# Performance work log

Measured on AMD Instinct MI355X. Metric: run time of the kernel, lower is better.

Reference implementation:

```python
import jax, jax.numpy as jnp
import numpy as np

N, E, F, H, C = 50000, 800000, 128, 256, 40
BN_EPS = 1e-5


def setup_inputs() -> dict:
    key = jax.random.key(0)
    ks = jax.random.split(key, 8)
    s = 0.05
    return {
        'x': jax.random.normal(ks[0], (N, F), jnp.float32),
        'edge_index': jax.random.randint(ks[1], (2, E), 0, N),
        'eps1': jnp.zeros((), jnp.float32),
        'W1': jax.random.normal(ks[2], (F, H), jnp.float32) * s,
        'b1': jnp.zeros((H,), jnp.float32),
        'g1': jnp.ones((H,), jnp.float32),
        'be1': jnp.zeros((H,), jnp.float32),
        'W2': jax.random.normal(ks[3], (H, H), jnp.float32) * s,
        'b2': jnp.zeros((H,), jnp.float32),
        'eps2': jnp.zeros((), jnp.float32),
        'W3': jax.random.normal(ks[4], (H, H), jnp.float32) * s,
        'b3': jnp.zeros((H,), jnp.float32),
        'g2': jnp.ones((H,), jnp.float32),
        'be2': jnp.zeros((H,), jnp.float32),
        'W4': jax.random.normal(ks[5], (H, H), jnp.float32) * s,
        'b4': jnp.zeros((H,), jnp.float32),
        'g3': jnp.ones((H,), jnp.float32),
        'be3': jnp.zeros((H,), jnp.float32),
        'Wf': jax.random.normal(ks[6], (H, C), jnp.float32) * s,
        'bf': jnp.zeros((C,), jnp.float32),
    }


def _bn(h, g, b):
    # BatchNorm1d forward with batch statistics (training-mode math, biased var)
    m = jnp.mean(h, axis=0)
    v = jnp.var(h, axis=0)
    return (h - m) * jax.lax.rsqrt(v + BN_EPS) * g + b


def _gin_conv(x, edge_index, eps, Wa, ba, g, be, Wb, bb):
    # GINConv: out = mlp((1+eps)*x + sum_{(src->dst)} x[src])
    src, dst = edge_index[0], edge_index[1]
    agg = jax.ops.segment_sum(x[src], dst, num_segments=x.shape[0])  # [N, d]
    h = (1.0 + eps) * x + agg
    h = jnp.maximum(_bn(h @ Wa + ba, g, be), 0.0)  # Linear-BN-ReLU
    return h @ Wb + bb                              # Linear


def reference(x, edge_index, eps1, W1, b1, g1, be1, W2, b2,
              eps2, W3, b3, g2, be2, W4, b4, g3, be3, Wf, bf):
    h = _gin_conv(x, edge_index, eps1, W1, b1, g1, be1, W2, b2)
    h = jnp.maximum(h, 0.0)  # F.relu (dropout p=0)
    h = _gin_conv(h, edge_index, eps2, W3, b3, g2, be2, W4, b4)
    h = jnp.maximum(_bn(h, g3, be3), 0.0)  # bn2 + relu
    return h @ Wf + bf  # fc -> [N, C]
```

## Files before the change

kernel.cpp:

```cpp
#include <hip/hip_runtime.h>
#include <hip/hip_bf16.h>


#define NN 50000
#define EE 800000
#define FDIM 128
#define HDIM 256
#define CDIM 40
#define BN_EPS 1e-5f

typedef unsigned short u16;
typedef unsigned int u32;
typedef __attribute__((ext_vector_type(8))) short short8;
typedef __attribute__((ext_vector_type(4))) float f32x4;

__device__ __forceinline__ float bflo(u32 u) { return __uint_as_float(u << 16); }
__device__ __forceinline__ float bfhi(u32 u) { return __uint_as_float(u & 0xFFFF0000u); }
__device__ __forceinline__ u16 f2bf(float f) {
  __hip_bfloat16 h = __float2bfloat16(f);
  return *(u16*)&h;
}
__device__ __forceinline__ u32 pack2(float a, float b) {
  return (u32)f2bf(a) | ((u32)f2bf(b) << 16);
}

__global__ void k_hist(const int* __restrict__ ei, int* __restrict__ deg) {
  int e = blockIdx.x * 256 + threadIdx.x;
  if (e < EE) atomicAdd(&deg[ei[EE + e]], 1);
}

__global__ void k_scan_blocks(const int* __restrict__ in, int* __restrict__ partial,
                              int* __restrict__ bsums, int n) {
  __shared__ int s[256];
  int i = blockIdx.x * 256 + threadIdx.x;
  s[threadIdx.x] = (i < n) ? in[i] : 0;
  __syncthreads();
  for (int d = 1; d < 256; d <<= 1) {
    int t = (threadIdx.x >= d) ? s[threadIdx.x - d] : 0;
    __syncthreads();
    s[threadIdx.x] += t;
    __syncthreads();
  }
  if (i < n) partial[i] = s[threadIdx.x];
  if (threadIdx.x == 255) bsums[blockIdx.x] = s[255];
}

__global__ void k_scan_sums(int* __restrict__ bs, int nb) {
  __shared__ int s[256];
  s[threadIdx.x] = (threadIdx.x < nb) ? bs[threadIdx.x] : 0;
  __syncthreads();
  for (int d = 1; d < 256; d <<= 1) {
    int t = (threadIdx.x >= d) ? s[threadIdx.x - d] : 0;
    __syncthreads();
    s[threadIdx.x] += t;
    __syncthreads();
  }
  int ex = (threadIdx.x == 0) ? 0 : s[threadIdx.x - 1];
  if (threadIdx.x < nb) bs[threadIdx.x] = ex;
}

__global__ void k_scan_add(const int* __restrict__ partial, const int* __restrict__ bs,
                           const int* __restrict__ deg,
                           int* __restrict__ rowstart, int* __restrict__ cursor, int n) {
  int i = blockIdx.x * 256 + threadIdx.x;
  if (i < n) {
    int incl = partial[i] + bs[blockIdx.x];
    rowstart[i + 1] = incl;
    cursor[i] = incl - deg[i];
  }
  if (i == 0) rowstart[0] = 0;
}

__global__ void k_scatter(const int* __restrict__ ei, int* __restrict__ cursor,
                          int* __restrict__ sorted_src) {
  int e = blockIdx.x * 256 + threadIdx.x;
  if (e < EE) {
    int dst = ei[EE + e];
    int p = atomicAdd(&cursor[dst], 1);
    sorted_src[p] = ei[e];
  }
}

__global__ void k_cvt_x(const float* __restrict__ x, u16* __restrict__ xb,
                        int* __restrict__ deg, float* __restrict__ stats) {
  int i = blockIdx.x * 256 + threadIdx.x;
  if (i < NN) deg[i] = 0;
  if (i < 6 * 256) stats[i] = 0.f;
  size_t base = (size_t)i * 4;
  if (base < (size_t)NN * FDIM) {
    float4 v = *(const float4*)&x[base];
    *(uint2*)&xb[base] = make_uint2(pack2(v.x, v.y), pack2(v.z, v.w));
  }
}

__global__ void k_cvt_w(const float* __restrict__ W1, const float* __restrict__ W2,
                        const float* __restrict__ W3, const float* __restrict__ W4,
                        const float* __restrict__ Wf,
                        u16* __restrict__ W1t, u16* __restrict__ W2t,
                        u16* __restrict__ W3t, u16* __restrict__ W4t,
                        u16* __restrict__ Wft) {
  int b = blockIdx.x, t = threadIdx.x;
  if (b < 128) {
    int i = b * 256 + t; int k = i >> 8, n = i & 255;
    W1t[(size_t)n * 128 + (((k >> 3) ^ (n & 7)) << 3) + (k & 7)] = f2bf(W1[i]);
  } else if (b < 384) {
    int i = (b - 128) * 256 + t; int k = i >> 8, n = i & 255;
    W2t[(size_t)n * 256 + (((k >> 3) ^ (n & 7)) << 3) + (k & 7)] = f2bf(W2[i]);
  } else if (b < 640) {
    int i = (b - 384) * 256 + t; int k = i >> 8, n = i & 255;
    W3t[(size_t)n * 256 + (((k >> 3) ^ (n & 7)) << 3) + (k & 7)] = f2bf(W3[i]);
  } else if (b < 896) {
    int i = (b - 640) * 256 + t; int k = i >> 8, n = i & 255;
    W4t[(size_t)n * 256 + (((k >> 3) ^ (n & 7)) << 3) + (k & 7)] = f2bf(W4[i]);
  } else {
    int j = (b - 896) * 256 + t;
    int c = j >> 8, k = j & 255;
    float v = (c < CDIM) ? Wf[(size_t)k * CDIM + c] : 0.f;
    Wft[(size_t)c * 256 + (((k >> 3) ^ (c & 7)) << 3) + (k & 7)] = f2bf(v);
  }
}

__global__ __launch_bounds__(256)
void k_agg1(const u16* __restrict__ x, const int* __restrict__ rowstart,
            const int* __restrict__ sorted_src, const float* __restrict__ epsp,
            u16* __restrict__ out) {
  int node = blockIdx.x * 4 + (threadIdx.x >> 6);
  if (node >= NN) return;
  int lane = threadIdx.x & 63;
  float e1 = 1.0f + epsp[0];
  int s = rowstart[node], t = rowstart[node + 1];
  const u32* xp = (const u32*)x;
  u32 u = xp[(size_t)node * 64 + lane];
  float a0 = bflo(u) * e1, a1 = bfhi(u) * e1;
  int p = s;
  for (; p + 7 < t; p += 8) {
    u32 uu[8];
#pragma unroll
    for (int i = 0; i < 8; ++i) uu[i] = xp[(size_t)sorted_src[p + i] * 64 + lane];
#pragma unroll
    for (int i = 0; i < 8; ++i) { a0 += bflo(uu[i]); a1 += bfhi(uu[i]); }
  }
  for (; p < t; ++p) {
    u32 u0 = xp[(size_t)sorted_src[p] * 64 + lane];
    a0 += bflo(u0); a1 += bfhi(u0);
  }
  ((u32*)out)[(size_t)node * 64 + lane] = pack2(a0, a1);
}

__global__ __launch_bounds__(256)
void k_agg2(const u16* __restrict__ x, const int* __restrict__ rowstart,
            const int* __restrict__ sorted_src, const float* __restrict__ epsp,
            u16* __restrict__ out) {
  int b = blockIdx.x;
  int h = (b & 7) >= 4;
  int tile = (b >> 3) * 4 + (b & 3);
  int node = tile * 4 + (threadIdx.x >> 6);
  if (node >= NN) return;
  int lane = threadIdx.x & 63;
  int off = h * 64 + lane;
  float e1 = 1.0f + epsp[0];
  int s = rowstart[node], t = rowstart[node + 1];
  const u32* xp = (const u32*)x;
  u32 u = xp[(size_t)node * 128 + off];
  float a0 = bflo(u) * e1, a1 = bfhi(u) * e1;
  int p = s;
  for (; p + 7 < t; p += 8) {
    u32 uu[8];
#pragma unroll
    for (int i = 0; i < 8; ++i) uu[i] = xp[(size_t)sorted_src[p + i] * 128 + off];
#pragma unroll
    for (int i = 0; i < 8; ++i) { a0 += bflo(uu[i]); a1 += bfhi(uu[i]); }
  }
  for (; p < t; ++p) {
    u32 u0 = xp[(size_t)sorted_src[p] * 128 + off];
    a0 += bflo(u0); a1 += bfhi(u0);
  }
  ((u32*)out)[(size_t)node * 128 + off] = pack2(a0, a1);
}

template <int K, bool TRANSFORM, bool RELU_OUT, bool COLSUMS>
__global__ __launch_bounds__(256, 4)
void k_gemm(const u16* __restrict__ A, const u16* __restrict__ Wt,
            const float* __restrict__ bias,
            const float* __restrict__ icsum, const float* __restrict__ icsq,
            const float* __restrict__ g, const float* __restrict__ be,
            u16* __restrict__ C, float* __restrict__ ocsum, float* __restrict__ ocsq) {
  __shared__ u16 SMEM[128 * 128];
  __shared__ float2 Tb[TRANSFORM ? 256 : 1];
  u16* Asm = SMEM;
  u16* Bsm = SMEM + 128 * 64;

  const int tid = threadIdx.x;
  const int lane = tid & 63;
  const int w = tid >> 6;
  const int wm = w >> 1, wn = w & 1;
  const int lr = lane & 15, lq = lane >> 4;
  const int r0 = (blockIdx.x >> 1) * 128;
  const int n0 = (blockIdx.x & 1) * 128;

  if constexpr (TRANSFORM) {
    float m = icsum[tid] * (1.0f / NN);
    float var = icsq[tid] * (1.0f / NN) - m * m;
    float s = g[tid] * rsqrtf(var + BN_EPS);
    Tb[tid] = make_float2(s, be[tid] - m * s);
    __syncthreads();
  }

  f32x4 acc[4][4];
#pragma unroll
  for (int mi = 0; mi < 4; ++mi)
#pragma unroll
    for (int ni = 0; ni < 4; ++ni) acc[mi][ni] = (f32x4){0.f, 0.f, 0.f, 0.f};

  const int srow = tid >> 3;
  const int sc = tid & 7;

  for (int k0 = 0; k0 < K; k0 += 64) {
    if (k0 > 0) __syncthreads();
#pragma unroll
    for (int it = 0; it < 4; ++it) {
      int row = it * 32 + srow;
      int gr = r0 + row;
      int grc = gr < NN ? gr : NN - 1;
      short8 va = *(const short8*)&A[(size_t)grc * K + k0 + sc * 8];
      if constexpr (TRANSFORM) {
#pragma unroll
        for (int j = 0; j < 8; ++j) {
          float2 tb = Tb[k0 + sc * 8 + j];
          float f = fmaxf(fmaf(__uint_as_float(((u32)(u16)va[j]) << 16), tb.x, tb.y), 0.f);
          va[j] = (short)f2bf(f);
        }
      }
      ((short8*)Asm)[row * 8 + (sc ^ (row & 7))] = va;
      short8 vb = *(const short8*)&Wt[(size_t)(n0 + row) * K + k0 + sc * 8];
      ((short8*)Bsm)[row * 8 + sc] = vb;
    }
    __syncthreads();

#pragma unroll
    for (int ks = 0; ks < 2; ++ks) {
      short8 af[4], bfx[4];
#pragma unroll
      for (int mi = 0; mi < 4; ++mi) {
        int row = wm * 64 + mi * 16 + lr;
        af[mi] = ((const short8*)Asm)[row * 8 + ((ks * 4 + lq) ^ (row & 7))];
      }
#pragma unroll
      for (int ni = 0; ni < 4; ++ni) {
        int rn = wn * 64 + ni * 16 + lr;
        bfx[ni] = ((const short8*)Bsm)[rn * 8 + ((ks * 4 + lq) ^ (rn & 7))];
      }
#pragma unroll
      for (int mi = 0; mi < 4; ++mi)
#pragma unroll
        for (int ni = 0; ni < 4; ++ni)
          acc[mi][ni] = __builtin_amdgcn_mfma_f32_16x16x32_bf16(af[mi], bfx[ni], acc[mi][ni], 0, 0, 0);
    }
  }
  __syncthreads();

  float bv[4];
#pragma unroll
  for (int ni = 0; ni < 4; ++ni) bv[ni] = bias[n0 + wn * 64 + ni * 16 + lr];
  float colS[4] = {}, colQ[4] = {};

  u16* Cs = SMEM;
#pragma unroll
  for (int mi = 0; mi < 4; ++mi)
#pragma unroll
    for (int ni = 0; ni < 4; ++ni) {
      int col = wn * 64 + ni * 16 + lr;
#pragma unroll
      for (int j = 0; j < 4; ++j) {
        int row = wm * 64 + mi * 16 + lq * 4 + j;
        float v = acc[mi][ni][j] + bv[ni];
        if constexpr (RELU_OUT) v = fmaxf(v, 0.f);
        if constexpr (COLSUMS) {
          if (r0 + row < NN) { colS[ni] += v; colQ[ni] += v * v; }
        }
        Cs[row * 128 + col] = f2bf(v);
      }
    }
  __syncthreads();

#pragma unroll
  for (int p = 0; p < 4; ++p) {
    int row = p * 32 + (tid >> 3);
    int gr = r0 + row;
    if (gr < NN) {
      int co = (tid & 7) * 16;
      *(uint4*)&C[(size_t)gr * 256 + n0 + co] = *(const uint4*)&Cs[row * 128 + co];
      *(uint4*)&C[(size_t)gr * 256 + n0 + co + 8] = *(const uint4*)&Cs[row * 128 + co + 8];
    }
  }

  if constexpr (COLSUMS) {
#pragma unroll
    for (int ni = 0; ni < 4; ++ni) {
      float s = colS[ni], q = colQ[ni];
      s += __shfl_xor(s, 16); s += __shfl_xor(s, 32);
      q += __shfl_xor(q, 16); q += __shfl_xor(q, 32);
      if (lq == 0) {
        int col = n0 + wn * 64 + ni * 16 + lr;
        atomicAdd(&ocsum[col], s);
        atomicAdd(&ocsq[col], q);
      }
    }
  }
}

__global__ __launch_bounds__(512)
void k_final(const u16* __restrict__ z3, const u16* __restrict__ Wft,
             const float* __restrict__ bfp,
             const float* __restrict__ icsum, const float* __restrict__ icsq,
             const float* __restrict__ g, const float* __restrict__ be,
             float* __restrict__ out) {
  __shared__ u16 Bs[48 * 256];
  __shared__ float2 Tb[256];
  const int tid = threadIdx.x;
  const int lane = tid & 63;
  const int w = tid >> 6;
  const int lr = lane & 15, lq = lane >> 4;
  const int r0 = blockIdx.x * 128;

  int row = r0 + w * 16 + lr;
  int rc = row < NN ? row : NN - 1;
  const u16* Ap = &z3[(size_t)rc * 256];
  short8 a[8];
#pragma unroll
  for (int ks = 0; ks < 8; ++ks)
    a[ks] = *(const short8*)&Ap[(ks * 4 + lq) * 8];

  {
    const short8* Bv = (const short8*)Wft;
    short8* Bl = (short8*)Bs;
#pragma unroll
    for (int i = 0; i < 3; ++i)
      Bl[tid + i * 512] = Bv[tid + i * 512];
  }
  if (tid < 256) {
    float m = icsum[tid] * (1.0f / NN);
    float var = icsq[tid] * (1.0f / NN) - m * m;
    float s = g[tid] * rsqrtf(var + BN_EPS);
    Tb[tid] = make_float2(s, be[tid] - m * s);
  }
  __syncthreads();

  f32x4 acc[3];
#pragma unroll
  for (int ni = 0; ni < 3; ++ni) acc[ni] = (f32x4){0.f, 0.f, 0.f, 0.f};
#pragma unroll
  for (int ks = 0; ks < 8; ++ks) {
    short8 t0 = a[ks];
    int kb = (ks * 4 + lq) * 8;
#pragma unroll
    for (int j = 0; j < 8; ++j) {
      float2 tb = Tb[kb + j];
      float f0 = fmaxf(fmaf(__uint_as_float(((u32)(u16)t0[j]) << 16), tb.x, tb.y), 0.f);
      t0[j] = (short)f2bf(f0);
    }
#pragma unroll
    for (int ni = 0; ni < 3; ++ni) {
      int col = ni * 16 + lr;
      short8 bfr = *(const short8*)&Bs[(size_t)col * 256 + (((ks * 4 + lq) ^ (col & 7)) << 3)];
      acc[ni] = __builtin_amdgcn_mfma_f32_16x16x32_bf16(t0, bfr, acc[ni], 0, 0, 0);
    }
  }

#pragma unroll
  for (int ni = 0; ni < 3; ++ni) {
    int col = ni * 16 + lr;
    if (col < CDIM) {
      float bfv = bfp[col];
#pragma unroll
      for (int j = 0; j < 4; ++j) {
        int gr = r0 + w * 16 + lq * 4 + j;
        if (gr < NN) out[(size_t)gr * CDIM + col] = acc[ni][j] + bfv;
      }
    }
  }
}

extern "C" void kernel_launch(void* const* d_in, const int* in_sizes, int n_in,
                              void* d_out, int out_size, void* d_ws, size_t ws_size,
                              hipStream_t stream) {
  const float* x   = (const float*)d_in[0];
  const int*   ei  = (const int*)d_in[1];
  const float* eps1= (const float*)d_in[2];
  const float* W1  = (const float*)d_in[3];
  const float* b1  = (const float*)d_in[4];
  const float* g1  = (const float*)d_in[5];
  const float* be1 = (const float*)d_in[6];
  const float* W2  = (const float*)d_in[7];
  const float* b2  = (const float*)d_in[8];
  const float* eps2= (const float*)d_in[9];
  const float* W3  = (const float*)d_in[10];
  const float* b3  = (const float*)d_in[11];
  const float* g2  = (const float*)d_in[12];
  const float* be2 = (const float*)d_in[13];
  const float* W4  = (const float*)d_in[14];
  const float* b4  = (const float*)d_in[15];
  const float* g3  = (const float*)d_in[16];
  const float* be3 = (const float*)d_in[17];
  const float* Wf  = (const float*)d_in[18];
  const float* bf  = (const float*)d_in[19];
  float* out = (float*)d_out;

  char* p = (char*)d_ws;
  auto alloc = [&](size_t bytes) -> char* {
    char* r = p;
    p += (bytes + 255) & ~(size_t)255;
    return r;
  };
  float* stats   = (float*)alloc(6 * 256 * sizeof(float));
  int* deg       = (int*)alloc(NN * sizeof(int));
  int* rowstart  = (int*)alloc((NN + 16) * sizeof(int));
  int* cursor    = (int*)alloc(NN * sizeof(int));
  int* sorted    = (int*)alloc(EE * sizeof(int));
  int* partial   = (int*)alloc(NN * sizeof(int));
  int* bsums     = (int*)alloc(1024 * sizeof(int));
  u16* W1t       = (u16*)alloc(256 * 128 * sizeof(u16));
  u16* W2t       = (u16*)alloc(256 * 256 * sizeof(u16));
  u16* W3t       = (u16*)alloc(256 * 256 * sizeof(u16));
  u16* W4t       = (u16*)alloc(256 * 256 * sizeof(u16));
  u16* Wft       = (u16*)alloc(48 * 256 * sizeof(u16));
  u16* xb        = (u16*)alloc((size_t)NN * 128 * sizeof(u16));
  u16* A1        = (u16*)alloc((size_t)NN * 128 * sizeof(u16));
  u16* z1        = (u16*)alloc((size_t)NN * 256 * sizeof(u16));
  u16* h1        = (u16*)alloc((size_t)NN * 256 * sizeof(u16));
  u16* A2        = (u16*)alloc((size_t)NN * 256 * sizeof(u16));
  (void)alloc(64 * 1024);
  u16* z2 = z1;
  u16* z3 = h1;

  float* s1 = stats + 0,    *q1 = stats + 256;
  float* s2 = stats + 512,  *q2 = stats + 768;
  float* s3 = stats + 1024, *q3 = stats + 1280;

  const int nbE = (EE + 255) / 256;
  const int nbN = (NN + 255) / 256;

  k_cvt_x<<<(NN * FDIM / 4 + 255) / 256, 256, 0, stream>>>(x, xb, deg, stats);
  k_cvt_w<<<944, 256, 0, stream>>>(W1, W2, W3, W4, Wf, W1t, W2t, W3t, W4t, Wft);
  k_hist<<<nbE, 256, 0, stream>>>(ei, deg);
  k_scan_blocks<<<nbN, 256, 0, stream>>>(deg, partial, bsums, NN);
  k_scan_sums<<<1, 256, 0, stream>>>(bsums, nbN);
  k_scan_add<<<nbN, 256, 0, stream>>>(partial, bsums, deg, rowstart, cursor, NN);
  k_scatter<<<nbE, 256, 0, stream>>>(ei, cursor, sorted);

  const int gGemm = ((NN + 127) / 128) * 2;

  k_agg1<<<(NN + 3) / 4, 256, 0, stream>>>(xb, rowstart, sorted, eps1, A1);
  k_gemm<128, false, false, true><<<gGemm, 256, 0, stream>>>(
      A1, W1t, b1, nullptr, nullptr, nullptr, nullptr, z1, s1, q1);
  k_gemm<256, true, true, false><<<gGemm, 256, 0, stream>>>(
      z1, W2t, b2, s1, q1, g1, be1, h1, nullptr, nullptr);

  k_agg2<<<((NN + 15) / 16) * 8, 256, 0, stream>>>(h1, rowstart, sorted, eps2, A2);
  k_gemm<256, false, false, true><<<gGemm, 256, 0, stream>>>(
      A2, W3t, b3, nullptr, nullptr, nullptr, nullptr, z2, s2, q2);
  k_gemm<256, true, false, true><<<gGemm, 256, 0, stream>>>(
      z2, W4t, b4, s2, q2, g2, be2, z3, s3, q3);

  k_final<<<(NN + 127) / 128, 512, 0, stream>>>(z3, Wft, bf, s3, q3, g3, be3, out);
}
```

Measured before the change: 372.0 us.

## Widen GEMM tile to full 256 columns and gather 8-byte rows in layer-2 aggregation

```diff
diff --git a/kernel.cpp b/kernel.cpp
--- a/kernel.cpp
+++ b/kernel.cpp
@@ -120,72 +120,66 @@
   }
 }
 
+template <int FEAT>
 __global__ __launch_bounds__(256)
-void k_agg1(const u16* __restrict__ x, const int* __restrict__ rowstart,
-            const int* __restrict__ sorted_src, const float* __restrict__ epsp,
-            u16* __restrict__ out) {
+void k_agg(const u16* __restrict__ x, const int* __restrict__ rowstart,
+           const int* __restrict__ sorted_src, const float* __restrict__ epsp,
+           u16* __restrict__ out) {
   int node = blockIdx.x * 4 + (threadIdx.x >> 6);
   if (node >= NN) return;
   int lane = threadIdx.x & 63;
   float e1 = 1.0f + epsp[0];
   int s = rowstart[node], t = rowstart[node + 1];
-  const u32* xp = (const u32*)x;
-  u32 u = xp[(size_t)node * 64 + lane];
-  float a0 = bflo(u) * e1, a1 = bfhi(u) * e1;
-  int p = s;
-  for (; p + 7 < t; p += 8) {
-    u32 uu[8];
-#pragma unroll
-    for (int i = 0; i < 8; ++i) uu[i] = xp[(size_t)sorted_src[p + i] * 64 + lane];
-#pragma unroll
-    for (int i = 0; i < 8; ++i) { a0 += bflo(uu[i]); a1 += bfhi(uu[i]); }
-  }
-  for (; p < t; ++p) {
-    u32 u0 = xp[(size_t)sorted_src[p] * 64 + lane];
-    a0 += bflo(u0); a1 += bfhi(u0);
-  }
-  ((u32*)out)[(size_t)node * 64 + lane] = pack2(a0, a1);
-}
-
-__global__ __launch_bounds__(256)
-void k_agg2(const u16* __restrict__ x, const int* __restrict__ rowstart,
-            const int* __restrict__ sorted_src, const float* __restrict__ epsp,
-            u16* __restrict__ out) {
-  int b = blockIdx.x;
-  int h = (b & 7) >= 4;
-  int tile = (b >> 3) * 4 + (b & 3);
-  int node = tile * 4 + (threadIdx.x >> 6);
-  if (node >= NN) return;
-  int lane = threadIdx.x & 63;
-  int off = h * 64 + lane;
-  float e1 = 1.0f + epsp[0];
-  int s = rowstart[node], t = rowstart[node + 1];
-  const u32* xp = (const u32*)x;
-  u32 u = xp[(size_t)node * 128 + off];
-  float a0 = bflo(u) * e1, a1 = bfhi(u) * e1;
-  int p = s;
-  for (; p + 7 < t; p += 8) {
-    u32 uu[8];
-#pragma unroll
-    for (int i = 0; i < 8; ++i) uu[i] = xp[(size_t)sorted_src[p + i] * 128 + off];
-#pragma unroll
-    for (int i = 0; i < 8; ++i) { a0 += bflo(uu[i]); a1 += bfhi(uu[i]); }
-  }
-  for (; p < t; ++p) {
-    u32 u0 = xp[(size_t)sorted_src[p] * 128 + off];
-    a0 += bflo(u0); a1 += bfhi(u0);
-  }
-  ((u32*)out)[(size_t)node * 128 + off] = pack2(a0, a1);
+  if constexpr (FEAT == 128) {
+    const u32* xp = (const u32*)x;
+    u32 u = xp[(size_t)node * 64 + lane];
+    float a0 = bflo(u) * e1, a1 = bfhi(u) * e1;
+    int p = s;
+    for (; p + 7 < t; p += 8) {
+      u32 uu[8];
+#pragma unroll
+      for (int i = 0; i < 8; ++i) uu[i] = xp[(size_t)sorted_src[p + i] * 64 + lane];
+#pragma unroll
+      for (int i = 0; i < 8; ++i) { a0 += bflo(uu[i]); a1 += bfhi(uu[i]); }
+    }
+    for (; p < t; ++p) {
+      u32 u0 = xp[(size_t)sorted_src[p] * 64 + lane];
+      a0 += bflo(u0); a1 += bfhi(u0);
+    }
+    ((u32*)out)[(size_t)node * 64 + lane] = pack2(a0, a1);
+  } else {
+    const uint2* xp = (const uint2*)x;
+    uint2 u = xp[(size_t)node * 64 + lane];
+    float a0 = bflo(u.x) * e1, a1 = bfhi(u.x) * e1;
+    float a2 = bflo(u.y) * e1, a3 = bfhi(u.y) * e1;
+    int p = s;
+    for (; p + 7 < t; p += 8) {
+      uint2 uu[8];
+#pragma unroll
+      for (int i = 0; i < 8; ++i) uu[i] = xp[(size_t)sorted_src[p + i] * 64 + lane];
+#pragma unroll
+      for (int i = 0; i < 8; ++i) {
+        a0 += bflo(uu[i].x); a1 += bfhi(uu[i].x);
+        a2 += bflo(uu[i].y); a3 += bfhi(uu[i].y);
+      }
+    }
+    for (; p < t; ++p) {
+      uint2 u0 = xp[(size_t)sorted_src[p] * 64 + lane];
+      a0 += bflo(u0.x); a1 += bfhi(u0.x);
+      a2 += bflo(u0.y); a3 += bfhi(u0.y);
+    }
+    ((uint2*)out)[(size_t)node * 64 + lane] = make_uint2(pack2(a0, a1), pack2(a2, a3));
+  }
 }
 
 template <int K, bool TRANSFORM, bool RELU_OUT, bool COLSUMS>
-__global__ __launch_bounds__(256, 4)
+__global__ __launch_bounds__(512, 4)
 void k_gemm(const u16* __restrict__ A, const u16* __restrict__ Wt,
             const float* __restrict__ bias,
             const float* __restrict__ icsum, const float* __restrict__ icsq,
             const float* __restrict__ g, const float* __restrict__ be,
             u16* __restrict__ C, float* __restrict__ ocsum, float* __restrict__ ocsq) {
-  __shared__ u16 SMEM[128 * 128];
+  __shared__ u16 SMEM[128 * 64 + 256 * 64];
   __shared__ float2 Tb[TRANSFORM ? 256 : 1];
   u16* Asm = SMEM;
   u16* Bsm = SMEM + 128 * 64;
@@ -193,16 +187,17 @@
   const int tid = threadIdx.x;
   const int lane = tid & 63;
   const int w = tid >> 6;
-  const int wm = w >> 1, wn = w & 1;
+  const int wm = w >> 2, wn = w & 3;
   const int lr = lane & 15, lq = lane >> 4;
-  const int r0 = (blockIdx.x >> 1) * 128;
-  const int n0 = (blockIdx.x & 1) * 128;
+  const int r0 = blockIdx.x * 128;
 
   if constexpr (TRANSFORM) {
-    float m = icsum[tid] * (1.0f / NN);
-    float var = icsq[tid] * (1.0f / NN) - m * m;
-    float s = g[tid] * rsqrtf(var + BN_EPS);
-    Tb[tid] = make_float2(s, be[tid] - m * s);
+    if (tid < 256) {
+      float m = icsum[tid] * (1.0f / NN);
+      float var = icsq[tid] * (1.0f / NN) - m * m;
+      float s = g[tid] * rsqrtf(var + BN_EPS);
+      Tb[tid] = make_float2(s, be[tid] - m * s);
+    }
     __syncthreads();
   }
 
@@ -218,8 +213,8 @@
   for (int k0 = 0; k0 < K; k0 += 64) {
     if (k0 > 0) __syncthreads();
 #pragma unroll
-    for (int it = 0; it < 4; ++it) {
-      int row = it * 32 + srow;
+    for (int it = 0; it < 2; ++it) {
+      int row = it * 64 + srow;
       int gr = r0 + row;
       int grc = gr < NN ? gr : NN - 1;
       short8 va = *(const short8*)&A[(size_t)grc * K + k0 + sc * 8];
@@ -232,7 +227,11 @@
         }
       }
       ((short8*)Asm)[row * 8 + (sc ^ (row & 7))] = va;
-      short8 vb = *(const short8*)&Wt[(size_t)(n0 + row) * K + k0 + sc * 8];
+    }
+#pragma unroll
+    for (int it = 0; it < 4; ++it) {
+      int row = it * 64 + srow;
+      short8 vb = *(const short8*)&Wt[(size_t)row * K + k0 + sc * 8];
       ((short8*)Bsm)[row * 8 + sc] = vb;
     }
     __syncthreads();
@@ -261,37 +260,42 @@
 
   float bv[4];
 #pragma unroll
-  for (int ni = 0; ni < 4; ++ni) bv[ni] = bias[n0 + wn * 64 + ni * 16 + lr];
+  for (int ni = 0; ni < 4; ++ni) bv[ni] = bias[wn * 64 + ni * 16 + lr];
   float colS[4] = {}, colQ[4] = {};
 
   u16* Cs = SMEM;
 #pragma unroll
-  for (int mi = 0; mi < 4; ++mi)
-#pragma unroll
-    for (int ni = 0; ni < 4; ++ni) {
-      int col = wn * 64 + ni * 16 + lr;
-#pragma unroll
-      for (int j = 0; j < 4; ++j) {
-        int row = wm * 64 + mi * 16 + lq * 4 + j;
-        float v = acc[mi][ni][j] + bv[ni];
-        if constexpr (RELU_OUT) v = fmaxf(v, 0.f);
-        if constexpr (COLSUMS) {
-          if (r0 + row < NN) { colS[ni] += v; colQ[ni] += v * v; }
+  for (int r = 0; r < 2; ++r) {
+    if (wm == r) {
+#pragma unroll
+      for (int mi = 0; mi < 4; ++mi)
+#pragma unroll
+        for (int ni = 0; ni < 4; ++ni) {
+          int col = wn * 64 + ni * 16 + lr;
+#pragma unroll
+          for (int j = 0; j < 4; ++j) {
+            int lrow = mi * 16 + lq * 4 + j;
+            float v = acc[mi][ni][j] + bv[ni];
+            if constexpr (RELU_OUT) v = fmaxf(v, 0.f);
+            if constexpr (COLSUMS) {
+              if (r0 + r * 64 + lrow < NN) { colS[ni] += v; colQ[ni] += v * v; }
+            }
+            Cs[lrow * 256 + col] = f2bf(v);
+          }
         }
-        Cs[row * 128 + col] = f2bf(v);
-      }
-    }
-  __syncthreads();
-
-#pragma unroll
-  for (int p = 0; p < 4; ++p) {
-    int row = p * 32 + (tid >> 3);
-    int gr = r0 + row;
-    if (gr < NN) {
-      int co = (tid & 7) * 16;
-      *(uint4*)&C[(size_t)gr * 256 + n0 + co] = *(const uint4*)&Cs[row * 128 + co];
-      *(uint4*)&C[(size_t)gr * 256 + n0 + co + 8] = *(const uint4*)&Cs[row * 128 + co + 8];
-    }
+    }
+    __syncthreads();
+    {
+      int lrow = tid >> 3;
+      int gr = r0 + r * 64 + lrow;
+      if (gr < NN) {
+        int co = (tid & 7) * 32;
+#pragma unroll
+        for (int i = 0; i < 4; ++i)
+          *(uint4*)&C[(size_t)gr * 256 + co + i * 8] = *(const uint4*)&Cs[lrow * 256 + co + i * 8];
+      }
+    }
+    __syncthreads();
   }
 
   if constexpr (COLSUMS) {
@@ -301,7 +305,7 @@
       s += __shfl_xor(s, 16); s += __shfl_xor(s, 32);
       q += __shfl_xor(q, 16); q += __shfl_xor(q, 32);
       if (lq == 0) {
-        int col = n0 + wn * 64 + ni * 16 + lr;
+        int col = wn * 64 + ni * 16 + lr;
         atomicAdd(&ocsum[col], s);
         atomicAdd(&ocsq[col], q);
       }
@@ -448,18 +452,18 @@
   k_scan_add<<<nbN, 256, 0, stream>>>(partial, bsums, deg, rowstart, cursor, NN);
   k_scatter<<<nbE, 256, 0, stream>>>(ei, cursor, sorted);
 
-  const int gGemm = ((NN + 127) / 128) * 2;
-
-  k_agg1<<<(NN + 3) / 4, 256, 0, stream>>>(xb, rowstart, sorted, eps1, A1);
-  k_gemm<128, false, false, true><<<gGemm, 256, 0, stream>>>(
+  const int gGemm = (NN + 127) / 128;
+
+  k_agg<128><<<(NN + 3) / 4, 256, 0, stream>>>(xb, rowstart, sorted, eps1, A1);
+  k_gemm<128, false, false, true><<<gGemm, 512, 0, stream>>>(
       A1, W1t, b1, nullptr, nullptr, nullptr, nullptr, z1, s1, q1);
-  k_gemm<256, true, true, false><<<gGemm, 256, 0, stream>>>(
+  k_gemm<256, true, true, false><<<gGemm, 512, 0, stream>>>(
       z1, W2t, b2, s1, q1, g1, be1, h1, nullptr, nullptr);
 
-  k_agg2<<<((NN + 15) / 16) * 8, 256, 0, stream>>>(h1, rowstart, sorted, eps2, A2);
-  k_gemm<256, false, false, true><<<gGemm, 256, 0, stream>>>(
+  k_agg<256><<<(NN + 3) / 4, 256, 0, stream>>>(h1, rowstart, sorted, eps2, A2);
+  k_gemm<256, false, false, true><<<gGemm, 512, 0, stream>>>(
       A2, W3t, b3, nullptr, nullptr, nullptr, nullptr, z2, s2, q2);
-  k_gemm<256, true, false, true><<<gGemm, 256, 0, stream>>>(
+  k_gemm<256, true, false, true><<<gGemm, 512, 0, stream>>>(
       z2, W4t, b4, s2, q2, g2, be2, z3, s3, q3);
 
   k_final<<<(NN + 127) / 128, 512, 0, stream>>>(z3, Wft, bf, s3, q3, g3, be3, out);
```

Result: faster. 336.3 us (-9.6%).
